# Kernel optimization log

Measured on AMD Instinct MI355X. Metric: run time of the kernel, lower is better.

Reference implementation:

```python
import jax, jax.numpy as jnp
import numpy as np

N_NODES = 100000
IN_F = 256
OUT_F = 256
BATCH = 50000
NUM_SAMPLES = 25


def setup_inputs() -> dict:
    key = jax.random.key(0)
    k1, k2, k3, k4 = jax.random.split(key, 4)
    features = jax.random.normal(k1, (N_NODES, IN_F), dtype=jnp.float32)
    node_idx = jax.random.randint(k2, (BATCH,), 0, N_NODES, dtype=jnp.int64 if jax.config.jax_enable_x64 else jnp.int32)
    neigh_idx = jax.random.randint(k3, (BATCH, NUM_SAMPLES), 0, N_NODES, dtype=jnp.int64 if jax.config.jax_enable_x64 else jnp.int32)
    # Linear(2*in_features, out_features, bias=False); torch stores weight as [out, 2*in],
    # we store W as [out, 2*in] transposed to [2*in, out] for x @ W.
    init_range = np.sqrt(6.0 / (2 * IN_F + OUT_F))
    W = jax.random.uniform(k4, (OUT_F, 2 * IN_F), dtype=jnp.float32, minval=-init_range, maxval=init_range)
    return {"features": features, "node_idx": node_idx, "neigh_idx": neigh_idx, "W": W}


def reference(features, node_idx, neigh_idx, W):
    # self features: [B, in]
    self_feat = features[node_idx]
    # gather + mean over sampled neighbors: [B, S, in] -> [B, in]
    neigh_mean = jnp.mean(features[neigh_idx], axis=1)
    # concat and project: [B, 2*in] @ [2*in, out]
    combined = jnp.concatenate([self_feat, neigh_mean], axis=1)
    return combined @ W.T
```

## Files before the change

kernel.cpp:

```cpp
#include <hip/hip_runtime.h>

#define N_NODES 100000
#define IN_F    256
#define OUT_F   256
#define BATCH   50000
#define NSAMP   25
#define K2      512
#define BR      64
#define BKH     128

typedef _Float16 f16_t;
typedef f16_t f16x8 __attribute__((ext_vector_type(8)));
typedef float f32x4 __attribute__((ext_vector_type(4)));
typedef float f32x2 __attribute__((ext_vector_type(2)));
typedef __bf16 bf16_t;
typedef bf16_t bf16x8 __attribute__((ext_vector_type(8)));

#if defined(__has_builtin)
#if __has_builtin(__builtin_amdgcn_cvt_pk_f32_fp8) && __has_builtin(__builtin_amdgcn_cvt_pk_fp8_f32)
#define FP8_HW 1
#endif
#endif
#ifndef FP8_HW
#include <hip/hip_fp8.h>
#endif

#define P8_OFF   51200000L
#define WG_OFF   76800000L
#define WS_NEED  (WG_OFF + 512L * 256 * 2)

typedef __attribute__((address_space(1))) const unsigned int gas_uint;
typedef __attribute__((address_space(3))) unsigned int las_uint;

__device__ __forceinline__ void gll16(const void* g, void* l) {
    __builtin_amdgcn_global_load_lds((gas_uint*)g, (las_uint*)l, 16, 0, 0);
}

__device__ __forceinline__ float h2f(unsigned short u) {
    union { unsigned short u; f16_t h; } t; t.u = u; return (float)t.h;
}

__device__ __forceinline__ unsigned int pk_fp8x4(float a, float b, float c, float d) {
#ifdef FP8_HW
    unsigned int r = __builtin_amdgcn_cvt_pk_fp8_f32(a, b, 0u, false);
    r = __builtin_amdgcn_cvt_pk_fp8_f32(c, d, r, true);
    return r;
#else
    union { unsigned char b[4]; unsigned int u; } t;
    t.b[0] = __hip_fp8_e4m3(a).__x; t.b[1] = __hip_fp8_e4m3(b).__x;
    t.b[2] = __hip_fp8_e4m3(c).__x; t.b[3] = __hip_fp8_e4m3(d).__x;
    return t.u;
#endif
}

__device__ __forceinline__ void acc_fp8x4(unsigned int v, float4& a) {
#ifdef FP8_HW
    f32x2 lo = __builtin_amdgcn_cvt_pk_f32_fp8(v, false);
    f32x2 hi = __builtin_amdgcn_cvt_pk_f32_fp8(v, true);
    a.x += lo[0]; a.y += lo[1]; a.z += hi[0]; a.w += hi[1];
#else
    union { unsigned int u; unsigned char b[4]; } t; t.u = v;
    __hip_fp8_e4m3 e0, e1, e2, e3;
    e0.__x = t.b[0]; e1.__x = t.b[1]; e2.__x = t.b[2]; e3.__x = t.b[3];
    a.x += (float)e0; a.y += (float)e1; a.z += (float)e2; a.w += (float)e3;
#endif
}

__global__ void wconv(const float* __restrict__ W, f16_t* __restrict__ Wg) {
    int idx = blockIdx.x * 256 + threadIdx.x;
    int j = idx >> 8, k = idx & 255;
    float v = (j < 256) ? W[j * K2 + k] : W[(j - 256) * K2 + 256 + k];
    Wg[idx] = (f16_t)v;
}

__global__ __launch_bounds__(256, 3) void proj_gemm(
    const float* __restrict__ features, const f16_t* __restrict__ Wg,
    f16_t* __restrict__ Pself, unsigned char* __restrict__ Pneigh8)
{
    __shared__ float          a32[BR * BKH];
    __shared__ unsigned short a16[BR * BKH];
    const int tid = threadIdx.x, lane = tid & 63, w = tid >> 6;
    const int q16 = lane >> 4, r16 = lane & 15;
    const long gr0 = (long)blockIdx.x * BR;
    const int c0g = blockIdx.y * 256 + w * 64;

    const f16_t* wbase = Wg + (long)(c0g + r16) * 256 + q16 * 8;

    f32x4 acc[4][4];
    #pragma unroll
    for (int ct = 0; ct < 4; ++ct)
        #pragma unroll
        for (int rt = 0; rt < 4; ++rt) acc[ct][rt] = (f32x4){0.f, 0.f, 0.f, 0.f};

    f16x8 wf[2][4];
    #pragma unroll
    for (int ct = 0; ct < 4; ++ct)
        wf[0][ct] = *(const f16x8*)(wbase + (long)ct * 16 * 256);

    #pragma unroll
    for (int i = 0; i < 8; ++i) {
        const int c   = i * 256 + tid;
        const int row = c >> 5, col16 = c & 31;
        long srow = gr0 + row; if (srow > N_NODES - 1) srow = N_NODES - 1;
        const int cbase = i * 256 + w * 64;
        gll16(&features[srow * IN_F + col16 * 4], &a32[cbase * 4]);
    }
    __syncthreads();

    #pragma unroll
    for (int h = 0; h < 2; ++h) {
        #pragma unroll
        for (int j = 0; j < 8; ++j) {
            const int q = tid + j * 256;
            const int row = q >> 5, c4 = (q & 31) * 4;
            const float4 f = *(const float4*)&a32[row * BKH + c4];
            union { ushort4 u; f16_t hh[4]; } t;
            t.hh[0] = (f16_t)f.x; t.hh[1] = (f16_t)f.y;
            t.hh[2] = (f16_t)f.z; t.hh[3] = (f16_t)f.w;
            *(ushort4*)&a16[row * BKH + (c4 ^ ((row & 7) << 3))] = t.u;
        }
        __syncthreads();

        if (h == 0) {
            #pragma unroll
            for (int i = 0; i < 8; ++i) {
                const int c   = i * 256 + tid;
                const int row = c >> 5, col16 = c & 31;
                long srow = gr0 + row; if (srow > N_NODES - 1) srow = N_NODES - 1;
                const int cbase = i * 256 + w * 64;
                gll16(&features[srow * IN_F + BKH + col16 * 4], &a32[cbase * 4]);
            }
        }

        #pragma unroll
        for (int sl = 0; sl < 4; ++sl) {
            const int sg = h * 4 + sl;
            if (sg < 7) {
                #pragma unroll
                for (int ct = 0; ct < 4; ++ct)
                    wf[(sg + 1) & 1][ct] =
                        *(const f16x8*)(wbase + (long)ct * 16 * 256 + (sg + 1) * 32);
            }
            f16x8 bfr[4];
            const int kc = sl * 32 + q16 * 8;
            #pragma unroll
            for (int rt = 0; rt < 4; ++rt) {
                const int row = rt * 16 + r16;
                bfr[rt] = *(const f16x8*)&a16[row * BKH + (kc ^ ((row & 7) << 3))];
            }
            #pragma unroll
            for (int ct = 0; ct < 4; ++ct)
                #pragma unroll
                for (int rt = 0; rt < 4; ++rt)
                    acc[ct][rt] = __builtin_amdgcn_mfma_f32_16x16x32_f16(
                        wf[sg & 1][ct], bfr[rt], acc[ct][rt], 0, 0, 0);
        }
        if (h == 0) __syncthreads();
    }

    if (blockIdx.y == 0) {
        #pragma unroll
        for (int rt = 0; rt < 4; ++rt) {
            const long row = gr0 + rt * 16 + r16;
            const bool ok = row < N_NODES;
            #pragma unroll
            for (int ct = 0; ct < 4; ++ct) {
                const int colb = w * 64 + ct * 16 + q16 * 4;
                if (ok) {
                    union { ushort4 u; f16_t hh[4]; } t;
                    t.hh[0] = (f16_t)acc[ct][rt][0]; t.hh[1] = (f16_t)acc[ct][rt][1];
                    t.hh[2] = (f16_t)acc[ct][rt][2]; t.hh[3] = (f16_t)acc[ct][rt][3];
                    *(ushort4*)&Pself[row * 256 + colb] = t.u;
                }
            }
        }
    } else {
        #pragma unroll
        for (int rt = 0; rt < 4; ++rt) {
            const long row = gr0 + rt * 16 + r16;
            const bool ok = row < N_NODES;
            #pragma unroll
            for (int ct = 0; ct < 4; ++ct) {
                const int colb = w * 64 + ct * 16 + q16 * 4;
                unsigned int pk = pk_fp8x4(acc[ct][rt][0], acc[ct][rt][1],
                                           acc[ct][rt][2], acc[ct][rt][3]);
                if (ok) *(unsigned int*)&Pneigh8[row * 256 + colb] = pk;
            }
        }
    }
}

__global__ __launch_bounds__(256) void gather_add(
    const f16_t* __restrict__ Pself, const unsigned char* __restrict__ P8,
    const int* __restrict__ node_idx, const int* __restrict__ neigh_idx,
    float* __restrict__ out)
{
    const int tid = threadIdx.x, lane = tid & 63, w = tid >> 6;
    const long b0 = (long)blockIdx.x * 8 + w * 2;
    const int c4 = lane * 4;

    int ns0[NSAMP], ns1[NSAMP];
    #pragma unroll
    for (int s = 0; s < NSAMP; ++s) ns0[s] = neigh_idx[b0 * NSAMP + s];
    #pragma unroll
    for (int s = 0; s < NSAMP; ++s) ns1[s] = neigh_idx[(b0 + 1) * NSAMP + s];
    const int sn0 = node_idx[b0], sn1 = node_idx[b0 + 1];

    const ushort4 sv0 = *(const ushort4*)&Pself[(long)sn0 * 256 + c4];
    const ushort4 sv1 = *(const ushort4*)&Pself[(long)sn1 * 256 + c4];

    unsigned int v0[NSAMP], v1[NSAMP];
    #pragma unroll
    for (int s = 0; s < NSAMP; ++s)
        v0[s] = *(const unsigned int*)&P8[(long)ns0[s] * 256 + c4];
    #pragma unroll
    for (int s = 0; s < NSAMP; ++s)
        v1[s] = *(const unsigned int*)&P8[(long)ns1[s] * 256 + c4];

    float4 a0 = make_float4(0.f, 0.f, 0.f, 0.f);
    float4 a1 = make_float4(0.f, 0.f, 0.f, 0.f);
    #pragma unroll
    for (int s = 0; s < NSAMP; ++s) acc_fp8x4(v0[s], a0);
    #pragma unroll
    for (int s = 0; s < NSAMP; ++s) acc_fp8x4(v1[s], a1);

    const float inv = 1.0f / (float)NSAMP;
    float4 o0, o1;
    o0.x = h2f(sv0.x) + a0.x * inv; o0.y = h2f(sv0.y) + a0.y * inv;
    o0.z = h2f(sv0.z) + a0.z * inv; o0.w = h2f(sv0.w) + a0.w * inv;
    o1.x = h2f(sv1.x) + a1.x * inv; o1.y = h2f(sv1.y) + a1.y * inv;
    o1.z = h2f(sv1.z) + a1.z * inv; o1.w = h2f(sv1.w) + a1.w * inv;
    *(float4*)&out[b0 * OUT_F + c4] = o0;
    *(float4*)&out[(b0 + 1) * OUT_F + c4] = o1;
}

__device__ __forceinline__ int swz_bf(int row, int us_idx) {
    return us_idx ^ ((row & 7) << 3);
}
__device__ __forceinline__ void store_bf4(unsigned short* comb, int r, int col, float4 f) {
    union { ushort4 u; bf16_t b[4]; } t;
    t.b[0] = (bf16_t)f.x; t.b[1] = (bf16_t)f.y;
    t.b[2] = (bf16_t)f.z; t.b[3] = (bf16_t)f.w;
    *(ushort4*)&comb[swz_bf(r, r * K2 + col)] = t.u;
}
__global__ __launch_bounds__(256, 4) void sage_fused(
    const float* __restrict__ features, const int* __restrict__ node_idx,
    const int* __restrict__ neigh_idx, const float* __restrict__ W,
    float* __restrict__ out)
{
    __shared__ unsigned short comb[16 * K2];
    const int tid = threadIdx.x, lane = tid & 63, wy = tid >> 6;
    const int b0 = blockIdx.x * 16;
    const int col4 = lane * 4;
    #pragma unroll
    for (int i = 0; i < 4; ++i) {
        const int r = wy * 4 + i;
        const long b = b0 + r;
        int nidx[NSAMP];
        #pragma unroll
        for (int s = 0; s < NSAMP; ++s) nidx[s] = neigh_idx[b * NSAMP + s];
        const int self_n = node_idx[b];
        const float4 sf = *(const float4*)&features[(long)self_n * IN_F + col4];
        float4 v[13];
        #pragma unroll
        for (int s = 0; s < 13; ++s)
            v[s] = *(const float4*)&features[(long)nidx[s] * IN_F + col4];
        float4 acc = v[0];
        #pragma unroll
        for (int s = 1; s < 13; ++s) {
            acc.x += v[s].x; acc.y += v[s].y; acc.z += v[s].z; acc.w += v[s].w;
        }
        #pragma unroll
        for (int s = 13; s < NSAMP; ++s)
            v[s - 13] = *(const float4*)&features[(long)nidx[s] * IN_F + col4];
        #pragma unroll
        for (int s = 0; s < 12; ++s) {
            acc.x += v[s].x; acc.y += v[s].y; acc.z += v[s].z; acc.w += v[s].w;
        }
        const float inv = 1.0f / (float)NSAMP;
        acc.x *= inv; acc.y *= inv; acc.z *= inv; acc.w *= inv;
        store_bf4(comb, r, col4, sf);
        store_bf4(comb, r, IN_F + col4, acc);
    }
    __syncthreads();
    const int c0 = wy * 64, arow = lane & 15, kq = (lane >> 4) * 8;
    f32x4 acc[4];
    #pragma unroll
    for (int t = 0; t < 4; ++t) acc[t] = (f32x4){0.f, 0.f, 0.f, 0.f};
    #pragma unroll
    for (int ks = 0; ks < 16; ++ks) {
        const int kb = ks * 32 + kq;
        const bf16x8 af = *(const bf16x8*)&comb[swz_bf(arow, arow * K2 + kb)];
        #pragma unroll
        for (int t = 0; t < 4; ++t) {
            const float* wp = &W[(long)(c0 + t * 16 + arow) * K2 + kb];
            const float4 w0 = *(const float4*)wp;
            const float4 w1 = *(const float4*)(wp + 4);
            bf16x8 bf;
            bf[0] = (bf16_t)w0.x; bf[1] = (bf16_t)w0.y;
            bf[2] = (bf16_t)w0.z; bf[3] = (bf16_t)w0.w;
            bf[4] = (bf16_t)w1.x; bf[5] = (bf16_t)w1.y;
            bf[6] = (bf16_t)w1.z; bf[7] = (bf16_t)w1.w;
            acc[t] = __builtin_amdgcn_mfma_f32_16x16x32_bf16(af, bf, acc[t], 0, 0, 0);
        }
    }
    #pragma unroll
    for (int t = 0; t < 4; ++t) {
        const int col = c0 + t * 16 + arow;
        #pragma unroll
        for (int j = 0; j < 4; ++j) {
            const int row = b0 + (lane >> 4) * 4 + j;
            out[(long)row * OUT_F + col] = acc[t][j];
        }
    }
}

extern "C" void kernel_launch(void* const* d_in, const int* in_sizes, int n_in,
                              void* d_out, int out_size, void* d_ws, size_t ws_size,
                              hipStream_t stream) {
    const float* features  = (const float*)d_in[0];
    const int*   node_idx  = (const int*)d_in[1];
    const int*   neigh_idx = (const int*)d_in[2];
    const float* W         = (const float*)d_in[3];
    float*       out       = (float*)d_out;

    if (ws_size >= (size_t)WS_NEED) {
        f16_t*         Pself  = (f16_t*)d_ws;
        unsigned char* P8     = (unsigned char*)d_ws + P8_OFF;
        f16_t*         Wg     = (f16_t*)((char*)d_ws + WG_OFF);
        wconv<<<512, 256, 0, stream>>>(W, Wg);
        proj_gemm<<<dim3(1563, 2), 256, 0, stream>>>(features, Wg, Pself, P8);
        gather_add<<<BATCH / 8, 256, 0, stream>>>(Pself, P8, node_idx, neigh_idx, out);
    } else {
        sage_fused<<<BATCH / 16, 256, 0, stream>>>(features, node_idx, neigh_idx, W, out);
    }
}
```

Baseline: 139.1 us.

## Make projection GEMM persistent with double-buffered async feature loads

The projection GEMM becomes a persistent kernel: 256x2 blocks loop over the 1563 row tiles, double-buffering fp32 feature halves in LDS so the next half-tile's global loads overlap the current MFMA work. The separate fp32-to-fp16 LDS conversion pass is dropped; conversion now happens in registers when the MFMA operands are read from an XOR-swizzled fp32 buffer. This removes a barrier and an LDS round-trip per half and hides load latency, but occupancy drops to 2 blocks per SIMD and the grid of 512 blocks may balance unevenly across CUs.

Measured after the change: 144.6 us. 3.9% more time.

```diff
diff --git a/kernel.cpp b/kernel.cpp
--- a/kernel.cpp
+++ b/kernel.cpp
@@ -6,8 +6,9 @@
 #define BATCH   50000
 #define NSAMP   25
 #define K2      512
-#define BR      64
 #define BKH     128
+#define NTILE   1563
+#define XS      256
 
 typedef _Float16 f16_t;
 typedef f16_t f16x8 __attribute__((ext_vector_type(8)));
@@ -73,121 +74,128 @@
     Wg[idx] = (f16_t)v;
 }
 
-__global__ __launch_bounds__(256, 3) void proj_gemm(
+__global__ __launch_bounds__(256, 2) void proj_gemm(
     const float* __restrict__ features, const f16_t* __restrict__ Wg,
     f16_t* __restrict__ Pself, unsigned char* __restrict__ Pneigh8)
 {
-    __shared__ float          a32[BR * BKH];
-    __shared__ unsigned short a16[BR * BKH];
+    __shared__ float buf[2][64 * BKH];
     const int tid = threadIdx.x, lane = tid & 63, w = tid >> 6;
     const int q16 = lane >> 4, r16 = lane & 15;
-    const long gr0 = (long)blockIdx.x * BR;
     const int c0g = blockIdx.y * 256 + w * 64;
 
     const f16_t* wbase = Wg + (long)(c0g + r16) * 256 + q16 * 8;
-
-    f32x4 acc[4][4];
-    #pragma unroll
-    for (int ct = 0; ct < 4; ++ct)
-        #pragma unroll
-        for (int rt = 0; rt < 4; ++rt) acc[ct][rt] = (f32x4){0.f, 0.f, 0.f, 0.f};
 
     f16x8 wf[2][4];
     #pragma unroll
     for (int ct = 0; ct < 4; ++ct)
         wf[0][ct] = *(const f16x8*)(wbase + (long)ct * 16 * 256);
 
-    #pragma unroll
-    for (int i = 0; i < 8; ++i) {
-        const int c   = i * 256 + tid;
-        const int row = c >> 5, col16 = c & 31;
-        long srow = gr0 + row; if (srow > N_NODES - 1) srow = N_NODES - 1;
-        const int cbase = i * 256 + w * 64;
-        gll16(&features[srow * IN_F + col16 * 4], &a32[cbase * 4]);
-    }
-    __syncthreads();
-
-    #pragma unroll
-    for (int h = 0; h < 2; ++h) {
-        #pragma unroll
-        for (int j = 0; j < 8; ++j) {
-            const int q = tid + j * 256;
-            const int row = q >> 5, c4 = (q & 31) * 4;
-            const float4 f = *(const float4*)&a32[row * BKH + c4];
-            union { ushort4 u; f16_t hh[4]; } t;
-            t.hh[0] = (f16_t)f.x; t.hh[1] = (f16_t)f.y;
-            t.hh[2] = (f16_t)f.z; t.hh[3] = (f16_t)f.w;
-            *(ushort4*)&a16[row * BKH + (c4 ^ ((row & 7) << 3))] = t.u;
-        }
-        __syncthreads();
-
-        if (h == 0) {
+    f32x4 acc[4][4];
+    #pragma unroll
+    for (int ct = 0; ct < 4; ++ct)
+        #pragma unroll
+        for (int rt = 0; rt < 4; ++rt) acc[ct][rt] = (f32x4){0.f, 0.f, 0.f, 0.f};
+
+#define STAGE(TT, HH, BSEL)                                                     \
+    {                                                                           \
+        const long gr_ = (long)(TT) * 64;                                       \
+        _Pragma("unroll")                                                       \
+        for (int i_ = 0; i_ < 8; ++i_) {                                        \
+            const int c_ = w * 8 + i_;             \
+            const int row_ = 2 * c_ + (lane >> 5);                              \
+            long srow_ = gr_ + row_; if (srow_ > N_NODES - 1) srow_ = N_NODES - 1; \
+            const int sg4_ = ((lane & 31) ^ (row_ & 7)) * 4;   \
+            gll16(&features[srow_ * IN_F + (HH) * BKH + sg4_],                  \
+                  &buf[BSEL][c_ * 256]);                                        \
+        }                                                                       \
+    }
+
+    STAGE(blockIdx.x, 0, 0);
+    int cur = 0;
+
+    for (int t = blockIdx.x; t < NTILE; t += XS) {
+        #pragma unroll
+        for (int h = 0; h < 2; ++h) {
+            __builtin_amdgcn_s_barrier();
+            const int nt = (h == 0) ? t : t + XS;
+            const bool hn = nt < NTILE;
+            if (hn) STAGE(nt, h ^ 1, cur ^ 1);
+            if (hn) asm volatile("s_waitcnt vmcnt(8)" ::: "memory");
+            else    asm volatile("s_waitcnt vmcnt(0)" ::: "memory");
+            __builtin_amdgcn_sched_barrier(0);
+            __builtin_amdgcn_s_barrier();
+
             #pragma unroll
-            for (int i = 0; i < 8; ++i) {
-                const int c   = i * 256 + tid;
-                const int row = c >> 5, col16 = c & 31;
-                long srow = gr0 + row; if (srow > N_NODES - 1) srow = N_NODES - 1;
-                const int cbase = i * 256 + w * 64;
-                gll16(&features[srow * IN_F + BKH + col16 * 4], &a32[cbase * 4]);
-            }
-        }
-
-        #pragma unroll
-        for (int sl = 0; sl < 4; ++sl) {
-            const int sg = h * 4 + sl;
-            if (sg < 7) {
+            for (int sl = 0; sl < 4; ++sl) {
+                const int sg = h * 4 + sl;
+                const int sn = (sg + 1) & 7;
                 #pragma unroll
                 for (int ct = 0; ct < 4; ++ct)
                     wf[(sg + 1) & 1][ct] =
-                        *(const f16x8*)(wbase + (long)ct * 16 * 256 + (sg + 1) * 32);
+                        *(const f16x8*)(wbase + (long)ct * 16 * 256 + sn * 32);
+                f16x8 bfr[4];
+                #pragma unroll
+                for (int rt = 0; rt < 4; ++rt) {
+                    const int row = rt * 16 + r16;
+                    const int lg0 = sl * 8 + q16 * 2;
+                    const float4 lo = *(const float4*)
+                        &buf[cur][row * BKH + ((lg0 ^ (row & 7)) << 2)];
+                    const float4 hi = *(const float4*)
+                        &buf[cur][row * BKH + (((lg0 + 1) ^ (row & 7)) << 2)];
+                    f16x8 bb;
+                    bb[0] = (f16_t)lo.x; bb[1] = (f16_t)lo.y;
+                    bb[2] = (f16_t)lo.z; bb[3] = (f16_t)lo.w;
+                    bb[4] = (f16_t)hi.x; bb[5] = (f16_t)hi.y;
+                    bb[6] = (f16_t)hi.z; bb[7] = (f16_t)hi.w;
+                    bfr[rt] = bb;
+                }
+                #pragma unroll
+                for (int ct = 0; ct < 4; ++ct)
+                    #pragma unroll
+                    for (int rt = 0; rt < 4; ++rt)
+                        acc[ct][rt] = __builtin_amdgcn_mfma_f32_16x16x32_f16(
+                            wf[sg & 1][ct], bfr[rt], acc[ct][rt], 0, 0, 0);
             }
-            f16x8 bfr[4];
-            const int kc = sl * 32 + q16 * 8;
+            cur ^= 1;
+        }
+
+        const long gr0 = (long)t * 64;
+        if (blockIdx.y == 0) {
             #pragma unroll
             for (int rt = 0; rt < 4; ++rt) {
-                const int row = rt * 16 + r16;
-                bfr[rt] = *(const f16x8*)&a16[row * BKH + (kc ^ ((row & 7) << 3))];
-            }
-            #pragma unroll
-            for (int ct = 0; ct < 4; ++ct)
-                #pragma unroll
-                for (int rt = 0; rt < 4; ++rt)
-                    acc[ct][rt] = __builtin_amdgcn_mfma_f32_16x16x32_f16(
-                        wf[sg & 1][ct], bfr[rt], acc[ct][rt], 0, 0, 0);
-        }
-        if (h == 0) __syncthreads();
-    }
-
-    if (blockIdx.y == 0) {
-        #pragma unroll
-        for (int rt = 0; rt < 4; ++rt) {
-            const long row = gr0 + rt * 16 + r16;
-            const bool ok = row < N_NODES;
-            #pragma unroll
-            for (int ct = 0; ct < 4; ++ct) {
-                const int colb = w * 64 + ct * 16 + q16 * 4;
-                if (ok) {
-                    union { ushort4 u; f16_t hh[4]; } t;
-                    t.hh[0] = (f16_t)acc[ct][rt][0]; t.hh[1] = (f16_t)acc[ct][rt][1];
-                    t.hh[2] = (f16_t)acc[ct][rt][2]; t.hh[3] = (f16_t)acc[ct][rt][3];
-                    *(ushort4*)&Pself[row * 256 + colb] = t.u;
+                const long row = gr0 + rt * 16 + r16;
+                const bool ok = row < N_NODES;
+                #pragma unroll
+                for (int ct = 0; ct < 4; ++ct) {
+                    const int colb = w * 64 + ct * 16 + q16 * 4;
+                    if (ok) {
+                        union { ushort4 u; f16_t hh[4]; } tt;
+                        tt.hh[0] = (f16_t)acc[ct][rt][0]; tt.hh[1] = (f16_t)acc[ct][rt][1];
+                        tt.hh[2] = (f16_t)acc[ct][rt][2]; tt.hh[3] = (f16_t)acc[ct][rt][3];
+                        *(ushort4*)&Pself[row * 256 + colb] = tt.u;
+                    }
                 }
             }
-        }
-    } else {
-        #pragma unroll
-        for (int rt = 0; rt < 4; ++rt) {
-            const long row = gr0 + rt * 16 + r16;
-            const bool ok = row < N_NODES;
+        } else {
             #pragma unroll
-            for (int ct = 0; ct < 4; ++ct) {
-                const int colb = w * 64 + ct * 16 + q16 * 4;
-                unsigned int pk = pk_fp8x4(acc[ct][rt][0], acc[ct][rt][1],
-                                           acc[ct][rt][2], acc[ct][rt][3]);
-                if (ok) *(unsigned int*)&Pneigh8[row * 256 + colb] = pk;
+            for (int rt = 0; rt < 4; ++rt) {
+                const long row = gr0 + rt * 16 + r16;
+                const bool ok = row < N_NODES;
+                #pragma unroll
+                for (int ct = 0; ct < 4; ++ct) {
+                    const int colb = w * 64 + ct * 16 + q16 * 4;
+                    unsigned int pk = pk_fp8x4(acc[ct][rt][0], acc[ct][rt][1],
+                                               acc[ct][rt][2], acc[ct][rt][3]);
+                    if (ok) *(unsigned int*)&Pneigh8[row * 256 + colb] = pk;
+                }
             }
         }
-    }
+        #pragma unroll
+        for (int ct = 0; ct < 4; ++ct)
+            #pragma unroll
+            for (int rt = 0; rt < 4; ++rt) acc[ct][rt] = (f32x4){0.f, 0.f, 0.f, 0.f};
+    }
+#undef STAGE
 }
 
 __global__ __launch_bounds__(256) void gather_add(
@@ -329,7 +337,7 @@
         unsigned char* P8     = (unsigned char*)d_ws + P8_OFF;
         f16_t*         Wg     = (f16_t*)((char*)d_ws + WG_OFF);
         wconv<<<512, 256, 0, stream>>>(W, Wg);
-        proj_gemm<<<dim3(1563, 2), 256, 0, stream>>>(features, Wg, Pself, P8);
+        proj_gemm<<<dim3(XS, 2), 256, 0, stream>>>(features, Wg, Pself, P8);
         gather_add<<<BATCH / 8, 256, 0, stream>>>(Pself, P8, node_idx, neigh_idx, out);
     } else {
         sage_fused<<<BATCH / 16, 256, 0, stream>>>(features, node_idx, neigh_idx, W, out);
```
